# Kernel optimization log

Measured on AMD Instinct MI355X. Metric: run time of the kernel, lower is better.

The kernel has to match this reference:

```python
import jax, jax.numpy as jnp
import numpy as np
from jax.scipy.special import gammaln

REG = 0.1  # reg_param from __init__


def setup_inputs() -> dict:
    key = jax.random.key(0)
    k1, k2 = jax.random.split(key)
    D, C, S, Q = 512, 64, 16, 2048  # feature_dim, n_way, shots, n_query
    X_support = jax.random.normal(k1, (C * S, D), dtype=jnp.float32)
    # balanced class labels (equivalent to argmax of a one-hot y)
    labels = jnp.arange(C * S, dtype=jnp.int32) % C
    X_query = jax.random.normal(k2, (Q, D), dtype=jnp.float32)
    # learned parameters, initialized exactly as in the torch module
    m = jnp.zeros((1, D), dtype=jnp.float32)
    kappa = jnp.asarray(0.1, dtype=jnp.float32)
    nu = jnp.asarray(float(D), dtype=jnp.float32)
    triu_diag = jnp.ones((D,), dtype=jnp.float32)
    triu_lower = jnp.eye(D, dtype=jnp.float32)
    return {"X_support": X_support, "labels": labels, "X_query": X_query,
            "m": m, "kappa": kappa, "nu": nu,
            "triu_diag": triu_diag, "triu_lower": triu_lower, "n_classes": 64}


def _forward(X_support, X_query, m, kappa, nu, triu_diag, triu_lower, labels, n_classes):
    N, D = X_support.shape
    C = int(n_classes)
    S = N // C  # balanced episode: N_j == S for every class

    # lower_triu = diag(|triu_diag|) + triu_lower * strictly_lower_mask
    mask = jnp.tril(jnp.ones((D, D), dtype=X_support.dtype), -1)
    L = jnp.diag(jnp.abs(triu_diag)) + triu_lower * mask

    kap = jnp.abs(kappa) + 1e-6
    nu_ = jnp.clip(nu, D - 1 + 1e-6)

    # group support samples by class: [C, S, D] (stable sort keeps per-class order)
    order = jnp.argsort(labels)
    Xg = X_support[order].reshape(C, S, D)
    Xmean = Xg.mean(axis=1)  # [C, D]

    # posterior means mu_j = kappa/(kappa+N) m + N/(kappa+N) mean(X_j)
    mu = (kap / (kap + S)) * m + (S / (kap + S)) * Xmean  # [C, D]

    # sum_outer(X_j) as one batched GEMM instead of a per-row loop
    XtX = jnp.einsum('csd,cse->cde', Xg, Xg)  # [C, D, D]
    base = L @ L.T + kap * (m.T @ m)          # [D, D], shared across classes
    S_ns = base[None] + XtX - (kap + S) * jnp.einsum('cd,ce->cde', mu, mu)
    sigma = S_ns * ((kap + S + 1.0) / ((nu_ + S - D + 1.0) * (kap + S)))  # [C, D, D]

    eye = jnp.eye(D, dtype=sigma.dtype)
    sigma_inv = (1.0 - REG) * jnp.linalg.inv(sigma) + REG * eye  # regularize()

    common = nu_ + S + 1.0 - D  # scalar (equal shots per class)
    _, logdet = jnp.linalg.slogdet(sigma)  # [C]
    bias = (gammaln(0.5 * (common + D)) - gammaln(0.5 * common)
            - 0.5 * D * jnp.log(common) - 0.5 * logdet)  # [C]

    # batched Mahalanobis distances: replaces nested python loops in predict()
    diff = X_query[None, :, :] - mu[:, None, :]              # [C, Q, D]
    t = jnp.einsum('cqd,cde->cqe', diff, sigma_inv)          # [C, Q, D]
    dist = jnp.sum(t * diff, axis=-1)                        # [C, Q]

    logits = bias[:, None] - 0.5 * (common + D) * jnp.log1p(dist / common)
    return logits.T  # [Q, C]


def reference(X_support, labels, X_query, m, kappa, nu, triu_diag, triu_lower, n_classes):
    return _forward(X_support, X_query, m, kappa, nu, triu_diag, triu_lower,
                    labels, n_classes)
```

## Files before the change

kernel.cpp:

```cpp
#include <hip/hip_runtime.h>
#include <math.h>

#define DD    512
#define CNUM  64
#define SHOTS 16
#define NSUP  1024
#define QNQ   2048
#define REGP  0.1f
#define XKS   4

typedef __attribute__((ext_vector_type(8))) short short8;
typedef __attribute__((ext_vector_type(4))) float f32x4;

__device__ __forceinline__ unsigned short f2bf(float f) {
  unsigned int u = __float_as_uint(f);
  unsigned int r = (u + 0x7fffu + ((u >> 16) & 1u)) >> 16;
  return (unsigned short)r;
}
__device__ __forceinline__ float bf2f(unsigned short h) {
  return __uint_as_float((unsigned int)h << 16);
}

static constexpr size_t OFF_W     = 0;
static constexpr size_t OFF_MU    = OFF_W     + 512*512;
static constexpr size_t OFF_Y     = OFF_MU    + 64*512;
static constexpr size_t OFF_Z     = OFF_Y     + 3136*512;
static constexpr size_t OFF_WM    = OFF_Z     + 3136;
static constexpr size_t OFF_CONST = OFF_WM    + 512;
static constexpr size_t OFF_IDX   = OFF_CONST + 16;
static constexpr size_t OFF_RMAP  = OFF_IDX   + 1024;
static constexpr size_t OFF_ZG    = OFF_RMAP  + 1088;
static constexpr size_t OFF_VMU   = OFF_ZG    + 1088;
static constexpr size_t OFF_MUBMU = OFF_VMU   + 1088;
static constexpr size_t OFF_MUN   = OFF_MUBMU + 64;
static constexpr size_t OFF_MINV  = OFF_MUN   + 64;
static constexpr size_t OFF_BIAS  = OFF_MINV  + 64*289;
static constexpr size_t OFF_QNRM  = OFF_BIAS  + 64;
static constexpr size_t OFF_YN    = OFF_QNRM  + 2048;
static constexpr size_t OFF_XMU   = OFF_YN    + 2048;
static constexpr size_t OFF_RG    = OFF_XMU   + (size_t)XKS*2048*64;
static constexpr size_t OFF_P     = OFF_RG    + 1088*2048;
static constexpr size_t OFF_PX    = OFF_P     + 3136*512;
static constexpr size_t OFF_PW    = OFF_PX    + 3136*512;


__global__ __launch_bounds__(256) void f_init(const float* tdiag, const float* tlow,
    const float* kappa, const float* nu, const int* labels, const float* Xs,
    const float* Xq, const float* m, float* W, float* cst, int* idx,
    int* rowmap, float* mu, float* mun,
    unsigned short* PX, unsigned short* PW) {
  __shared__ float sh[2 * 64 * 68 + 32 * 33];
  __shared__ int sidx[SHOTS];
  int b = blockIdx.x, tid = threadIdx.x;
  if (b == 0) {
    if (tid == 0) {
      float kap = fabsf(kappa[0]) + 1e-6f;
      float nu_ = fmaxf(nu[0], (float)(DD - 1) + 1e-6f);
      float common = nu_ + (float)SHOTS + 1.0f - (float)DD;
      float scale = (kap + SHOTS + 1.0f) / ((nu_ + SHOTS - DD + 1.0f) * (kap + SHOTS));
      cst[0] = kap;
      cst[1] = scale;
      cst[2] = common;
      cst[3] = 0.5f * (common + DD);
      cst[4] = lgammaf(0.5f * (common + DD)) - lgammaf(0.5f * common)
               - 0.5f * (float)DD * logf(common);
      cst[5] = -(kap + SHOTS);
      cst[6] = kap / (kap + SHOTS);
      cst[7] = 1.0f / (kap + SHOTS);
      cst[8] = (float)DD * logf(scale);
      cst[9] = -1.0f / (kap + SHOTS);
    }
  } else if (b < 65) {
    int c = b - 1;
    if (tid < 64) {
      int lane = tid, cnt = 0;
      for (int i0 = 0; i0 < NSUP; i0 += 64) {
        int lab = labels[i0 + lane];
        unsigned long long mm = __ballot(lab == c);
        if (lab == c) {
          int pos = cnt + __popcll(mm & ((1ull << lane) - 1ull));
          if (pos < SHOTS) idx[c * SHOTS + pos] = i0 + lane;
        }
        cnt += __popcll(mm);
      }
    }
    __syncthreads();
    if (tid < 17)
      rowmap[c * 17 + tid] = (tid < SHOTS) ? (QNQ + idx[c * SHOTS + tid])
                                           : (QNQ + NSUP + c);
  } else if (b < 129) {
    int c = b - 65;
    if (tid < 64) {
      int lane = tid, cnt = 0;
      for (int i0 = 0; i0 < NSUP; i0 += 64) {
        int lab = labels[i0 + lane];
        unsigned long long mm = __ballot(lab == c);
        if (lab == c) {
          int pos = cnt + __popcll(mm & ((1ull << lane) - 1ull));
          if (pos < SHOTS) sidx[pos] = i0 + lane;
        }
        cnt += __popcll(mm);
      }
    }
    __syncthreads();
    float kap = fabsf(kappa[0]) + 1e-6f;
    float cm = kap / (kap + SHOTS), cx = 1.0f / (kap + SHOTS);
    float* red = sh;
    float acc = 0.0f;
    size_t prow = (size_t)(3072 + c) * 1024;
    for (int d = tid; d < DD; d += 256) {
      float s = 0.0f;
      for (int sh_ = 0; sh_ < SHOTS; sh_++)
        s += Xs[(size_t)sidx[sh_] * DD + d];
      float v = cm * m[d] + cx * s;
      mu[(size_t)c * DD + d] = v;
      unsigned short h = f2bf(v), l = f2bf(v - bf2f(h));
      PX[prow + d] = h;
      PX[prow + 512 + d] = l;
      acc += v * v;
    }
    red[tid] = acc;
    __syncthreads();
    for (int off = 128; off > 0; off >>= 1) {
      if (tid < off) red[tid] += red[tid + off];
      __syncthreads();
    }
    if (tid == 0) mun[c] = red[0];
  } else if (b < 137) {
    int jb = b - 129;
    float* Ld = sh;
    float* Wd = sh + 64 * 68;
    float* tsh = sh + 2 * 64 * 68;
    for (int t = tid; t < 4096; t += 256) {
      int r = t >> 6, c = t & 63;
      int gr = jb * 64 + r;
      float v = (r == c) ? fabsf(tdiag[gr])
              : (r > c ? tlow[(size_t)gr * DD + jb * 64 + c] : 0.0f);
      Ld[r * 68 + c] = v;
      Wd[r * 68 + c] = 0.0f;
    }
    __syncthreads();
    if (tid < 64) {
      int s = tid >> 4, t = tid & 15;
      int r0 = s * 16;
      #pragma unroll
      for (int i = 0; i < 16; i++) {
        float w = (i == t) ? 1.0f : 0.0f;
        #pragma unroll
        for (int k = 0; k < 16; k++)
          if (k < i) w -= Ld[(r0 + i) * 68 + r0 + k] * Wd[(r0 + k) * 68 + r0 + t];
        Wd[(r0 + i) * 68 + r0 + t] = w / Ld[(r0 + i) * 68 + r0 + i];
      }
    }
    __syncthreads();
    for (int g2 = 0; g2 < 2; g2++) {
      int r0 = g2 * 32 + 16, c0 = g2 * 32;
      int rr = tid >> 4, cc = tid & 15;
      float t_ = 0.0f;
      #pragma unroll
      for (int k = 0; k < 16; k++)
        t_ += Ld[(r0 + rr) * 68 + c0 + k] * Wd[(c0 + k) * 68 + c0 + cc];
      tsh[rr * 33 + cc] = t_;
      __syncthreads();
      float x = 0.0f;
      #pragma unroll
      for (int k = 0; k < 16; k++)
        x -= Wd[(r0 + rr) * 68 + r0 + k] * tsh[k * 33 + cc];
      Wd[(r0 + rr) * 68 + c0 + cc] = x;
      __syncthreads();
    }
    {
      int rr = tid >> 6, cc = tid & 63;
      #pragma unroll
      for (int p = 0; p < 4; p++) {
        int r = rr + p * 4, c = cc;
        if (c < 32) {
          float t_ = 0.0f;
          #pragma unroll
          for (int k = 0; k < 32; k++)
            t_ += Ld[(32 + r) * 68 + k] * Wd[k * 68 + c];
          tsh[r * 33 + c] = t_;
        } else {
          int c2 = c - 32;
          float t_ = 0.0f;
          #pragma unroll
          for (int k = 0; k < 32; k++)
            t_ += Ld[(32 + r + 16) * 68 + k] * Wd[k * 68 + c2];
          tsh[(r + 16) * 33 + c2] = t_;
        }
      }
      __syncthreads();
      #pragma unroll
      for (int p = 0; p < 4; p++) {
        int r = rr + p * 4, c = cc;
        int r2 = (c < 32) ? r : r + 16;
        int c2 = (c < 32) ? c : c - 32;
        float x = 0.0f;
        #pragma unroll
        for (int k = 0; k < 32; k++)
          x -= Wd[(32 + r2) * 68 + 32 + k] * tsh[k * 33 + c2];
        Wd[(32 + r2) * 68 + c2] = x;
      }
    }
    __syncthreads();
    float* Wblk = W + (size_t)(jb * 64) * DD + jb * 64;
    for (int t = tid; t < 4096; t += 256) {
      int r = t >> 6, c = t & 63;
      float v = Wd[r * 68 + c];
      Wblk[(size_t)r * DD + c] = v;
      unsigned short h = f2bf(v), l = f2bf(v - bf2f(h));
      size_t prow = (size_t)(jb * 64 + r) * 1024 + jb * 64 + c;
      PW[prow] = h;
      PW[prow + 512] = l;
    }
  } else {
    int r0 = (b - 137) * 4;
    int row = r0 + (tid >> 6), lane = tid & 63;
    const float* src = (row < QNQ) ? Xq + (size_t)row * DD
                                   : Xs + (size_t)(row - QNQ) * DD;
    size_t prow = (size_t)row * 1024;
    #pragma unroll
    for (int p = 0; p < 2; p++) {
      int col = lane * 8 + p * 4;
      float4 v = *(const float4*)(src + col);
      ushort4 hi, lo;
      hi.x = f2bf(v.x); lo.x = f2bf(v.x - bf2f(hi.x));
      hi.y = f2bf(v.y); lo.y = f2bf(v.y - bf2f(hi.y));
      hi.z = f2bf(v.z); lo.z = f2bf(v.z - bf2f(hi.z));
      hi.w = f2bf(v.w); lo.w = f2bf(v.w - bf2f(hi.w));
      *(ushort4*)(PX + prow + col) = hi;
      *(ushort4*)(PX + prow + 512 + col) = lo;
    }
  }
}

__device__ __forceinline__ void tile_stage(float* S, const float* __restrict__ G, int ldg) {
  int tid = threadIdx.x;
  #pragma unroll
  for (int p = 0; p < 4; p++) {
    int f4 = tid + 256 * p;
    int row = f4 >> 4, c4 = (f4 & 15) * 4;
    *(float4*)&S[row * 68 + c4] = *(const float4*)(G + (size_t)row * ldg + c4);
  }
}
__device__ __forceinline__ void tile_fma(float acc[4][4], const float* As, const float* Bs) {
  int tid = threadIdx.x, tr = tid >> 4, tc = tid & 15;
  #pragma unroll
  for (int kk = 0; kk < 64; kk++) {
    float a[4];
    #pragma unroll
    for (int x = 0; x < 4; x++) a[x] = As[(tr * 4 + x) * 68 + kk];
    float4 bv = *(const float4*)&Bs[kk * 68 + tc * 4];
    float bb[4] = {bv.x, bv.y, bv.z, bv.w};
    #pragma unroll
    for (int x = 0; x < 4; x++)
      #pragma unroll
      for (int y = 0; y < 4; y++) acc[x][y] += a[x] * bb[y];
  }
}
__device__ __forceinline__ void tile_out_neg(const float acc[4][4], float* W,
    unsigned short* PW, int gr0, int gc0) {
  int tid = threadIdx.x, tr = tid >> 4, tc = tid & 15;
  #pragma unroll
  for (int x = 0; x < 4; x++) {
    #pragma unroll
    for (int y = 0; y < 4; y++) {
      float v = -acc[x][y];
      W[(size_t)(gr0 + tr * 4 + x) * DD + gc0 + tc * 4 + y] = v;
      unsigned short h = f2bf(v), l = f2bf(v - bf2f(h));
      size_t prow = (size_t)(gr0 + tr * 4 + x) * 1024 + gc0 + tc * 4 + y;
      PW[prow] = h;
      PW[prow + 512] = l;
    }
  }
}

#define GBK 16
__global__ __launch_bounds__(256) void k_m128_xmu(const float* __restrict__ tlow,
    const float* __restrict__ W_, float* __restrict__ Wout,
    const float* __restrict__ Xq, const float* __restrict__ Mu,
    float* __restrict__ xmup, unsigned short* __restrict__ PW) {
  __shared__ float sh[3 * 64 * 68];
  int b = blockIdx.x, tid = threadIdx.x;
  if (b < 4) {
    float* As = sh;
    float* Bs = sh + 64 * 68;
    float* tsh = sh + 2 * 64 * 68;
    int base = b * 128;
    float tacc[4][4] = {};
    tile_stage(As, tlow + (size_t)(base + 64) * DD + base, DD);
    tile_stage(Bs, W_ + (size_t)base * DD + base, DD);
    __syncthreads();
    tile_fma(tacc, As, Bs);
    __syncthreads();
    {
      int tr = tid >> 4, tc = tid & 15;
      #pragma unroll
      for (int x = 0; x < 4; x++)
        #pragma unroll
        for (int y = 0; y < 4; y++) tsh[(tr * 4 + x) * 68 + tc * 4 + y] = tacc[x][y];
    }
    tile_stage(As, W_ + (size_t)(base + 64) * DD + base + 64, DD);
    __syncthreads();
    float xacc[4][4] = {};
    tile_fma(xacc, As, tsh);
    tile_out_neg(xacc, Wout, PW, base + 64, base);
  } else {
    float* Ms = sh;
    float* Qs = sh + 64 * 68;
    int xb = b - 4;
    int bm = (xb & 63) * 32, kq = xb >> 6;
    int tr = tid >> 4, tc = tid & 15;
    float acc[4][2] = {};
    int k0s = kq * (DD / XKS), k0e = k0s + DD / XKS;
    for (int k0 = k0s; k0 < k0e; k0 += GBK) {
      {
        int row = tid >> 2, k4 = tid & 3;
        float4 v = *(const float4*)(Mu + (size_t)row * DD + k0 + k4 * 4);
        Ms[(k4 * 4 + 0) * 68 + row] = v.x; Ms[(k4 * 4 + 1) * 68 + row] = v.y;
        Ms[(k4 * 4 + 2) * 68 + row] = v.z; Ms[(k4 * 4 + 3) * 68 + row] = v.w;
      }
      if (tid < 128) {
        int row = tid >> 2, k4 = tid & 3;
        float4 v = *(const float4*)(Xq + (size_t)(bm + row) * DD + k0 + k4 * 4);
        Qs[(k4 * 4 + 0) * 36 + row] = v.x; Qs[(k4 * 4 + 1) * 36 + row] = v.y;
        Qs[(k4 * 4 + 2) * 36 + row] = v.z; Qs[(k4 * 4 + 3) * 36 + row] = v.w;
      }
      __syncthreads();
      #pragma unroll
      for (int kk = 0; kk < GBK; kk++) {
        float4 m0 = *(const float4*)&Ms[kk * 68 + tr * 4];
        float a[4] = {m0.x, m0.y, m0.z, m0.w};
        float q0 = Qs[kk * 36 + tc * 2], q1 = Qs[kk * 36 + tc * 2 + 1];
        #pragma unroll
        for (int y = 0; y < 4; y++) {
          acc[y][0] += a[y] * q0;
          acc[y][1] += a[y] * q1;
        }
      }
      __syncthreads();
    }
    #pragma unroll
    for (int y = 0; y < 4; y++) {
      float2 v = make_float2(acc[y][0], acc[y][1]);
      *(float2*)(xmup + ((size_t)kq * CNUM + tr * 4 + y) * QNQ + bm + tc * 2) = v;
    }
  }
}

__global__ __launch_bounds__(256) void k_m256(const float* __restrict__ tlow,
    float* __restrict__ W, unsigned short* __restrict__ PW) {
  __shared__ float sh[3 * 64 * 68];
  float* As = sh;
  float* Bs = sh + 64 * 68;
  float* tsh = sh + 2 * 64 * 68;
  int b = blockIdx.x, tid = threadIdx.x;
  int g = b >> 2, rem = b & 3, i = rem >> 1, j = rem & 1;
  int base = g * 256;
  float xacc[4][4] = {};
  for (int k = 0; k <= i; k++) {
    float tacc[4][4] = {};
    for (int l = j; l < 2; l++) {
      __syncthreads();
      tile_stage(As, tlow + (size_t)(base + 128 + 64 * k) * DD + base + 64 * l, DD);
      tile_stage(Bs, W + (size_t)(base + 64 * l) * DD + base + 64 * j, DD);
      __syncthreads();
      tile_fma(tacc, As, Bs);
    }
    __syncthreads();
    {
      int tr = tid >> 4, tc = tid & 15;
      #pragma unroll
      for (int x = 0; x < 4; x++)
        #pragma unroll
        for (int y = 0; y < 4; y++) tsh[(tr * 4 + x) * 68 + tc * 4 + y] = tacc[x][y];
    }
    tile_stage(As, W + (size_t)(base + 128 + 64 * i) * DD + base + 128 + 64 * k, DD);
    __syncthreads();
    tile_fma(xacc, As, tsh);
  }
  tile_out_neg(xacc, W, PW, base + 128 + 64 * i, base + 64 * j);
}

__device__ __forceinline__ void nn64_sh(float* As, float* Bs,
    const float* __restrict__ A, int lda, const float* __restrict__ B, int ldb,
    float* __restrict__ Cd, int ldc, int k0, int k1, float sgn,
    unsigned short* __restrict__ Pw, int gr0, int gc0) {
  int tid = threadIdx.x, tr = tid >> 4, tc = tid & 15;
  float acc[4][4] = {};
  for (int kc = k0; kc < k1; kc += 64) {
    #pragma unroll
    for (int p = 0; p < 4; p++) {
      int f4 = tid + 256 * p;
      int row = f4 >> 4, c4 = f4 & 15;
      *(float4*)&As[row * 68 + c4 * 4] = *(const float4*)(A + (size_t)row * lda + kc + c4 * 4);
      *(float4*)&Bs[row * 68 + c4 * 4] = *(const float4*)(B + (size_t)(kc + row) * ldb + c4 * 4);
    }
    __syncthreads();
    #pragma unroll
    for (int kk = 0; kk < 64; kk++) {
      float a[4];
      #pragma unroll
      for (int x = 0; x < 4; x++) a[x] = As[(tr * 4 + x) * 68 + kk];
      float4 bv = *(const float4*)&Bs[kk * 68 + tc * 4];
      float bb[4] = {bv.x, bv.y, bv.z, bv.w};
      #pragma unroll
      for (int x = 0; x < 4; x++)
        #pragma unroll
        for (int y = 0; y < 4; y++) acc[x][y] += a[x] * bb[y];
    }
    __syncthreads();
  }
  #pragma unroll
  for (int x = 0; x < 4; x++) {
    float4 v = make_float4(sgn * acc[x][0], sgn * acc[x][1],
                           sgn * acc[x][2], sgn * acc[x][3]);
    *(float4*)(Cd + (size_t)(tr * 4 + x) * ldc + tc * 4) = v;
    if (Pw) {
      size_t prow = (size_t)(gr0 + tr * 4 + x) * 1024 + gc0 + tc * 4;
      float vv[4] = {v.x, v.y, v.z, v.w};
      #pragma unroll
      for (int y = 0; y < 4; y++) {
        unsigned short h = f2bf(vv[y]), l = f2bf(vv[y] - bf2f(h));
        Pw[prow + y] = h;
        Pw[prow + 512 + y] = l;
      }
    }
  }
}

__global__ __launch_bounds__(256) void k_triT(const float* __restrict__ tlow,
                                              const float* __restrict__ W,
                                              float* __restrict__ T, int s) {
  __shared__ float sh[2 * 64 * 68];
  int h = s >> 1, tiles = h >> 6, per = tiles * tiles;
  int g = blockIdx.x / per, rem = blockIdx.x % per;
  int ti = rem / tiles, tj = rem % tiles;
  int base = g * s;
  const float* A = tlow + (size_t)(base + h + ti * 64) * DD + base;
  const float* B = W + (size_t)base * DD + base + tj * 64;
  float* Cd = T + (size_t)g * h * h + (size_t)(ti * 64) * h + tj * 64;
  nn64_sh(sh, sh + 64 * 68, A, DD, B, DD, Cd, h, tj * 64, h, 1.0f, nullptr, 0, 0);
}

__global__ __launch_bounds__(256) void k_triX(float* __restrict__ W,
                                              const float* __restrict__ T, int s,
                                              unsigned short* __restrict__ PW) {
  __shared__ float sh[2 * 64 * 68];
  int h = s >> 1, tiles = h >> 6, per = tiles * tiles;
  int g = blockIdx.x / per, rem = blockIdx.x % per;
  int ti = rem / tiles, tj = rem % tiles;
  int base = g * s;
  const float* A = W + (size_t)(base + h + ti * 64) * DD + base + h;
  const float* B = T + (size_t)g * h * h + tj * 64;
  int gr0 = base + h + ti * 64, gc0 = base + tj * 64;
  float* Cd = W + (size_t)gr0 * DD + gc0;
  nn64_sh(sh, sh + 64 * 68, A, DD, B, h, Cd, DD, 0, (ti + 1) * 64, -1.0f, PW, gr0, gc0);
}

#define PSTR 80
__global__ __launch_bounds__(256) void f_y_wm(const unsigned short* __restrict__ PX,
    const unsigned short* __restrict__ PW, const float* __restrict__ W,
    const float* __restrict__ m, float* __restrict__ Y,
    unsigned short* __restrict__ Pm, float* __restrict__ wm) {
  __shared__ unsigned short AshH[64 * PSTR];
  __shared__ unsigned short AshL[64 * PSTR];
  __shared__ unsigned short BshH[64 * PSTR];
  __shared__ unsigned short BshL[64 * PSTR];
  int b = blockIdx.x, tid = threadIdx.x;
  if (b < 392) {
    int mt = b >> 3, nt = b & 7;
    int bm = mt * 64, bn = nt * 64;
    int lane = tid & 63, wave = tid >> 6;
    int wr = wave >> 1, wc = wave & 1;
    int mrow = lane & 15, q = lane >> 4;
    f32x4 acc00 = {}, acc01 = {}, acc10 = {}, acc11 = {};
    int kchunks = nt + 1;
    for (int it = 0; it < kchunks; it++) {
      int kc = it * 64;
      #pragma unroll
      for (int p = 0; p < 2; p++) {
        int idx = tid + 256 * p;
        int row = idx >> 3, c8 = (idx & 7) * 8;
        *(short8*)&AshH[row * PSTR + c8] =
            *(const short8*)(PX + (size_t)(bm + row) * 1024 + kc + c8);
        *(short8*)&AshL[row * PSTR + c8] =
            *(const short8*)(PX + (size_t)(bm + row) * 1024 + 512 + kc + c8);
        *(short8*)&BshH[row * PSTR + c8] =
            *(const short8*)(PW + (size_t)(bn + row) * 1024 + kc + c8);
        *(short8*)&BshL[row * PSTR + c8] =
            *(const short8*)(PW + (size_t)(bn + row) * 1024 + 512 + kc + c8);
      }
      __syncthreads();
      #pragma unroll
      for (int ks = 0; ks < 2; ks++) {
        int ko = ks * 32 + q * 8;
        short8 ah0 = *(const short8*)&AshH[(wr * 32 + mrow) * PSTR + ko];
        short8 ah1 = *(const short8*)&AshH[(wr * 32 + 16 + mrow) * PSTR + ko];
        short8 al0 = *(const short8*)&AshL[(wr * 32 + mrow) * PSTR + ko];
        short8 al1 = *(const short8*)&AshL[(wr * 32 + 16 + mrow) * PSTR + ko];
        short8 bh0 = *(const short8*)&BshH[(wc * 32 + mrow) * PSTR + ko];
        short8 bh1 = *(const short8*)&BshH[(wc * 32 + 16 + mrow) * PSTR + ko];
        short8 bl0 = *(const short8*)&BshL[(wc * 32 + mrow) * PSTR + ko];
        short8 bl1 = *(const short8*)&BshL[(wc * 32 + 16 + mrow) * PSTR + ko];
        acc00 = __builtin_amdgcn_mfma_f32_16x16x32_bf16(ah0, bh0, acc00, 0, 0, 0);
        acc00 = __builtin_amdgcn_mfma_f32_16x16x32_bf16(ah0, bl0, acc00, 0, 0, 0);
        acc00 = __builtin_amdgcn_mfma_f32_16x16x32_bf16(al0, bh0, acc00, 0, 0, 0);
        acc00 = __builtin_amdgcn_mfma_f32_16x16x32_bf16(al0, bl0, acc00, 0, 0, 0);
        acc01 = __builtin_amdgcn_mfma_f32_16x16x32_bf16(ah0, bh1, acc01, 0, 0, 0);
        acc01 = __builtin_amdgcn_mfma_f32_16x16x32_bf16(ah0, bl1, acc01, 0, 0, 0);
        acc01 = __builtin_amdgcn_mfma_f32_16x16x32_bf16(al0, bh1, acc01, 0, 0, 0);
        acc01 = __builtin_amdgcn_mfma_f32_16x16x32_bf16(al0, bl1, acc01, 0, 0, 0);
        acc10 = __builtin_amdgcn_mfma_f32_16x16x32_bf16(ah1, bh0, acc10, 0, 0, 0);
        acc10 = __builtin_amdgcn_mfma_f32_16x16x32_bf16(ah1, bl0, acc10, 0, 0, 0);
        acc10 = __builtin_amdgcn_mfma_f32_16x16x32_bf16(al1, bh0, acc10, 0, 0, 0);
        acc10 = __builtin_amdgcn_mfma_f32_16x16x32_bf16(al1, bl0, acc10, 0, 0, 0);
        acc11 = __builtin_amdgcn_mfma_f32_16x16x32_bf16(ah1, bh1, acc11, 0, 0, 0);
        acc11 = __builtin_amdgcn_mfma_f32_16x16x32_bf16(ah1, bl1, acc11, 0, 0, 0);
        acc11 = __builtin_amdgcn_mfma_f32_16x16x32_bf16(al1, bh1, acc11, 0, 0, 0);
        acc11 = __builtin_amdgcn_mfma_f32_16x16x32_bf16(al1, bl1, acc11, 0, 0, 0);
      }
      __syncthreads();
    }
    #pragma unroll
    for (int r = 0; r < 4; r++) {
      int row0 = bm + wr * 32 + q * 4 + r;
      int row1 = row0 + 16;
      int col0 = bn + wc * 32 + mrow;
      float vv[4] = {acc00[r], acc01[r], acc10[r], acc11[r]};
      int rows[4] = {row0, row0, row1, row1};
      int cols[4] = {col0, col0 + 16, col0, col0 + 16};
      #pragma unroll
      for (int e = 0; e < 4; e++) {
        Y[(size_t)rows[e] * DD + cols[e]] = vv[e];
        unsigned short h = f2bf(vv[e]), l = f2bf(vv[e] - bf2f(h));
        Pm[(size_t)rows[e] * 1024 + cols[e]] = h;
        Pm[(size_t)rows[e] * 1024 + 512 + cols[e]] = l;
      }
    }
  } else {
    int wave = tid >> 6, lane = tid & 63;
    int row = (b - 392) * 4 + wave;
    float s = 0.0f;
    for (int j = lane; j <= row; j += 64) s += W[(size_t)row * DD + j] * m[j];
    for (int off = 32; off > 0; off >>= 1) s += __shfl_down(s, off);
    if (lane == 0) wm[row] = s;
  }
}

__global__ __launch_bounds__(256) void f_z_rg_gram(const unsigned short* __restrict__ Pm,
    const float* __restrict__ Y, const float* __restrict__ tdiag,
    const int* __restrict__ rowmap, const float* __restrict__ Xq,
    const float* __restrict__ wm, float* __restrict__ cst,
    float* __restrict__ Rg,
    float* __restrict__ z, float* __restrict__ qn, float* __restrict__ yn,
    float* __restrict__ zg, float* __restrict__ Vmu, float* __restrict__ muBmu,
    float* __restrict__ Minv, float* __restrict__ bias) {
  __shared__ float sh[9920];
  __shared__ int pivrow;
  __shared__ float detacc, csmS, ldbS;
  int b = blockIdx.x, tid = threadIdx.x;
  if (b < 544) {
    unsigned short* ush = (unsigned short*)sh;
    unsigned short* Ash = ush;
    unsigned short* Bsh = ush + 64 * PSTR;
    unsigned short* Csh = ush + 2 * 64 * PSTR;
    int bm = (b >> 5) * 64, bn = (b & 31) * 64;
    int lane = tid & 63, wave = tid >> 6;
    int wr = wave >> 1, wc = wave & 1;
    int mrow = lane & 15, q = lane >> 4;
    int srowA[2];
    #pragma unroll
    for (int p = 0; p < 2; p++) srowA[p] = rowmap[bm + ((tid + 256 * p) >> 3)];
    f32x4 acc00 = {}, acc01 = {}, acc10 = {}, acc11 = {};
    for (int it = 0; it < 16; it++) {
      int kc = it * 64;
      int kcX = kc ^ 512;
      #pragma unroll
      for (int p = 0; p < 2; p++) {
        int idx = tid + 256 * p;
        int row = idx >> 3, c8 = (idx & 7) * 8;
        *(short8*)&Ash[row * PSTR + c8] =
            *(const short8*)(Pm + (size_t)srowA[p] * 1024 + kc + c8);
        *(short8*)&Bsh[row * PSTR + c8] =
            *(const short8*)(Pm + (size_t)(bn + row) * 1024 + kc + c8);
        *(short8*)&Csh[row * PSTR + c8] =
            *(const short8*)(Pm + (size_t)(bn + row) * 1024 + kcX + c8);
      }
      __syncthreads();
      #pragma unroll
      for (int ks = 0; ks < 2; ks++) {
        int ko = ks * 32 + q * 8;
        short8 a0 = *(const short8*)&Ash[(wr * 32 + mrow) * PSTR + ko];
        short8 a1 = *(const short8*)&Ash[(wr * 32 + 16 + mrow) * PSTR + ko];
        short8 b0 = *(const short8*)&Bsh[(wc * 32 + mrow) * PSTR + ko];
        short8 b1 = *(const short8*)&Bsh[(wc * 32 + 16 + mrow) * PSTR + ko];
        short8 c0 = *(const short8*)&Csh[(wc * 32 + mrow) * PSTR + ko];
        short8 c1 = *(const short8*)&Csh[(wc * 32 + 16 + mrow) * PSTR + ko];
        acc00 = __builtin_amdgcn_mfma_f32_16x16x32_bf16(a0, b0, acc00, 0, 0, 0);
        acc01 = __builtin_amdgcn_mfma_f32_16x16x32_bf16(a0, b1, acc01, 0, 0, 0);
        acc10 = __builtin_amdgcn_mfma_f32_16x16x32_bf16(a1, b0, acc10, 0, 0, 0);
        acc11 = __builtin_amdgcn_mfma_f32_16x16x32_bf16(a1, b1, acc11, 0, 0, 0);
        acc00 = __builtin_amdgcn_mfma_f32_16x16x32_bf16(a0, c0, acc00, 0, 0, 0);
        acc01 = __builtin_amdgcn_mfma_f32_16x16x32_bf16(a0, c1, acc01, 0, 0, 0);
        acc10 = __builtin_amdgcn_mfma_f32_16x16x32_bf16(a1, c0, acc10, 0, 0, 0);
        acc11 = __builtin_amdgcn_mfma_f32_16x16x32_bf16(a1, c1, acc11, 0, 0, 0);
      }
      __syncthreads();
    }
    #pragma unroll
    for (int r = 0; r < 4; r++) {
      int row0 = bm + wr * 32 + q * 4 + r;
      int row1 = row0 + 16;
      int col0 = bn + wc * 32 + mrow;
      Rg[(size_t)row0 * QNQ + col0]      = acc00[r];
      Rg[(size_t)row0 * QNQ + col0 + 16] = acc01[r];
      Rg[(size_t)row1 * QNQ + col0]      = acc10[r];
      Rg[(size_t)row1 * QNQ + col0 + 16] = acc11[r];
    }
  } else if (b < 1056) {
    int wave = tid >> 6, lane = tid & 63;
    int row = (b - 544) * 4 + wave;
    const float* xr = Xq + (size_t)row * DD;
    const float* yr = Y + (size_t)row * DD;
    float sz = 0.0f, s1 = 0.0f, s2 = 0.0f;
    for (int j4 = lane; j4 < 128; j4 += 64) {
      float4 xv = *(const float4*)(xr + j4 * 4);
      float4 yv = *(const float4*)(yr + j4 * 4);
      float4 wv = *(const float4*)(wm + j4 * 4);
      sz += yv.x * wv.x + yv.y * wv.y + yv.z * wv.z + yv.w * wv.w;
      s1 += xv.x * xv.x + xv.y * xv.y + xv.z * xv.z + xv.w * xv.w;
      s2 += yv.x * yv.x + yv.y * yv.y + yv.z * yv.z + yv.w * yv.w;
    }
    for (int off = 32; off > 0; off >>= 1) {
      sz += __shfl_down(sz, off);
      s1 += __shfl_down(s1, off);
      s2 += __shfl_down(s2, off);
    }
    if (lane == 0) {
      z[row] = sz;
      qn[row] = s1;
      yn[row] = s2;
    }
  } else if (b == 1056) {
    float* red = sh;
    float* red2 = sh + 256;
    float a = 0.0f, l = 0.0f;
    for (int t = tid; t < DD; t += 256) {
      float w = wm[t]; a += w * w;
      l += logf(fabsf(tdiag[t]));
    }
    red[tid] = a; red2[tid] = l;
    __syncthreads();
    for (int off = 128; off > 0; off >>= 1) {
      if (tid < off) { red[tid] += red[tid + off]; red2[tid] += red2[tid + off]; }
      __syncthreads();
    }
    if (tid == 0) {
      float kap = cst[0], ss = red[0];
      cst[10] = kap / (1.0f + kap * ss);
      cst[11] = 2.0f * red2[0] + logf(1.0f + kap * ss);
    }
  } else {
    int c = b - 1057;
    float* red = sh;
    float* red2 = sh + 256;
    {
      float a = 0.0f, l = 0.0f;
      for (int t = tid; t < DD; t += 256) {
        float w = wm[t]; a += w * w;
        l += logf(fabsf(tdiag[t]));
      }
      red[tid] = a; red2[tid] = l;
      __syncthreads();
      for (int off = 128; off > 0; off >>= 1) {
        if (tid < off) { red[tid] += red[tid + off]; red2[tid] += red2[tid + off]; }
        __syncthreads();
      }
      if (tid == 0) {
        float kap = cst[0], ss = red[0];
        csmS = kap / (1.0f + kap * ss);
        ldbS = 2.0f * red2[0] + logf(1.0f + kap * ss);
      }
      __syncthreads();
    }
    float* Ys  = sh;
    float* aug = sh + 8772;
    float* zs  = aug + 595;
    float* colk = zs + 17;
    for (int t = tid; t < 17 * 128; t += 256) {
      int r = t >> 7, col = t & 127;
      *(float4*)&Ys[r * 516 + col * 4] =
          *(const float4*)(Y + (size_t)rowmap[c * 17 + r] * DD + col * 4);
    }
    __syncthreads();
    {
      int wave = tid >> 6, lane = tid & 63;
      for (int a = wave; a < 17; a += 4) {
        float s = 0.0f;
        for (int j = lane; j < DD; j += 64) s += Ys[a * 516 + j] * wm[j];
        for (int off = 32; off > 0; off >>= 1) s += __shfl_down(s, off);
        if (lane == 0) zs[a] = s;
      }
    }
    __syncthreads();
    float csm = csmS;
    for (int e = tid; e < 289; e += 256) {
      int a = e / 17, bb = e % 17;
      const float* ra = &Ys[a * 516];
      const float* rb = &Ys[bb * 516];
      float s = 0.0f;
      for (int k = 0; k < 128; k++) {
        float4 va = *(const float4*)&ra[k * 4];
        float4 vb = *(const float4*)&rb[k * 4];
        s += va.x * vb.x + va.y * vb.y + va.z * vb.z + va.w * vb.w;
      }
      float g = s - csm * zs[a] * zs[bb];
      if (a == bb) g += (a < 16) ? 1.0f : cst[9];
      aug[a * 35 + bb] = g;
      aug[a * 35 + 17 + bb] = (a == bb) ? 1.0f : 0.0f;
    }
    __syncthreads();
    if (tid < 17) {
      float gv = aug[tid * 35 + 16];
      if (tid == 16) gv -= cst[9];
      Vmu[c * 17 + tid] = gv;
      if (tid == 16) muBmu[c] = gv;
      zg[c * 17 + tid] = zs[tid];
    }
    if (tid == 0) detacc = 0.0f;
    __syncthreads();
    for (int k = 0; k < 17; k++) {
      if (tid == 0) {
        int p = k; float best = fabsf(aug[k * 35 + k]);
        for (int r = k + 1; r < 17; r++) {
          float v = fabsf(aug[r * 35 + k]);
          if (v > best) { best = v; p = r; }
        }
        pivrow = p;
      }
      __syncthreads();
      int p = pivrow;
      if (p != k) {
        for (int cc = tid; cc < 34; cc += 256) {
          float tmp = aug[k * 35 + cc]; aug[k * 35 + cc] = aug[p * 35 + cc]; aug[p * 35 + cc] = tmp;
        }
      }
      __syncthreads();
      if (tid == 0) detacc += logf(fabsf(aug[k * 35 + k]));
      if (tid < 17) colk[tid] = aug[tid * 35 + k];
      __syncthreads();
      float invp = 1.0f / aug[k * 35 + k];
      for (int cc = tid; cc < 34; cc += 256) aug[k * 35 + cc] *= invp;
      __syncthreads();
      for (int t = tid; t < 17 * 34; t += 256) {
        int r = t / 34, cc = t % 34;
        if (r != k) aug[r * 35 + cc] -= colk[r] * aug[k * 35 + cc];
      }
      __syncthreads();
    }
    for (int t = tid; t < 289; t += 256)
      Minv[(size_t)c * 289 + t] = aug[(t / 17) * 35 + 17 + t % 17];
    if (tid == 0) {
      float slog = logf(fabsf(cst[5])) + detacc;
      float logdetSigma = cst[8] + ldbS + slog;
      bias[c] = cst[4] - 0.5f * logdetSigma;
    }
  }
}

__global__ __launch_bounds__(256) void k_logits(const float* __restrict__ Rg,
    const float* z, const float* zg,
    const float* Vmu, const float* muBmu, const float* mun, const float* yn,
    const float* qn, const float* xmup, const float* Minv, const float* bias,
    const float* cst, float* out) {
  __shared__ float Ms[289], Vs[17], Zs[17];
  int c = blockIdx.y;
  int q = blockIdx.x * 256 + threadIdx.x;
  for (int t = threadIdx.x; t < 289; t += 256) Ms[t] = Minv[(size_t)c * 289 + t];
  if (threadIdx.x < 17) {
    Vs[threadIdx.x] = Vmu[c * 17 + threadIdx.x];
    Zs[threadIdx.x] = zg[c * 17 + threadIdx.x];
  }
  __syncthreads();
  float csm = cst[10], scale = cst[1], common = cst[2], coef = cst[3];
  float zq = z[q];
  float r[17];
  float xBmu = 0.0f;
  for (int a = 0; a < 17; a++) {
    float raw = Rg[(size_t)(c * 17 + a) * QNQ + q] - csm * Zs[a] * zq;
    if (a == 16) xBmu = raw;
    r[a] = raw - Vs[a];
  }
  float qB = yn[q] - csm * zq * zq;
  float quadB = qB - 2.0f * xBmu + muBmu[c];
  float corr = 0.0f;
  for (int a = 0; a < 17; a++) {
    float e = 0.0f;
    for (int bb = 0; bb < 17; bb++) e += Ms[a * 17 + bb] * r[bb];
    corr += r[a] * e;
  }
  float distB = (quadB - corr) / scale;
  float xm = 0.0f;
  #pragma unroll
  for (int p = 0; p < XKS; p++)
    xm += xmup[((size_t)(p * CNUM + c)) * QNQ + q];
  float dn = qn[q] - 2.0f * xm + mun[c];
  float dist = (1.0f - REGP) * distB + REGP * dn;
  out[(size_t)q * CNUM + c] = bias[c] - coef * log1pf(dist / common);
}

extern "C" void kernel_launch(void* const* d_in, const int* in_sizes, int n_in,
                              void* d_out, int out_size, void* d_ws, size_t ws_size,
                              hipStream_t stream) {
  const float* Xs    = (const float*)d_in[0];
  const int*   labels= (const int*)d_in[1];
  const float* Xq    = (const float*)d_in[2];
  const float* m     = (const float*)d_in[3];
  const float* kappa = (const float*)d_in[4];
  const float* nu    = (const float*)d_in[5];
  const float* tdiag = (const float*)d_in[6];
  const float* tlow  = (const float*)d_in[7];
  float* ws = (float*)d_ws;
  float* W    = ws + OFF_W;
  float* mu   = ws + OFF_MU;
  float* Y    = ws + OFF_Y;
  float* z    = ws + OFF_Z;
  float* wm   = ws + OFF_WM;
  float* cst  = ws + OFF_CONST;
  int*   idx  = (int*)(ws + OFF_IDX);
  int*   rmap = (int*)(ws + OFF_RMAP);
  float* zg   = ws + OFF_ZG;
  float* Vmu  = ws + OFF_VMU;
  float* muBmu= ws + OFF_MUBMU;
  float* mun  = ws + OFF_MUN;
  float* Minv = ws + OFF_MINV;
  float* bias = ws + OFF_BIAS;
  float* qn   = ws + OFF_QNRM;
  float* yn   = ws + OFF_YN;
  float* xmup = ws + OFF_XMU;
  float* Rg   = ws + OFF_RG;
  unsigned short* P  = (unsigned short*)(ws + OFF_P);
  unsigned short* PX = (unsigned short*)(ws + OFF_PX);
  unsigned short* PW = (unsigned short*)(ws + OFF_PW);
  float* Ttmp = ws + OFF_RG;
  float* out  = (float*)d_out;

  f_init<<<905, 256, 0, stream>>>(tdiag, tlow, kappa, nu, labels, Xs, Xq, m,
                                  W, cst, idx, rmap, mu, mun, PX, PW);
  k_m128_xmu<<<260, 256, 0, stream>>>(tlow, W, W, Xq, mu, xmup, PW);
  k_m256<<<8, 256, 0, stream>>>(tlow, W, PW);
  k_triT<<<16, 256, 0, stream>>>(tlow, W, Ttmp, 512);
  k_triX<<<16, 256, 0, stream>>>(W, Ttmp, 512, PW);
  f_y_wm<<<520, 256, 0, stream>>>(PX, PW, W, m, Y, P, wm);
  f_z_rg_gram<<<544 + 512 + 1 + 64, 256, 0, stream>>>(P, Y, tdiag, rmap, Xq, wm,
                                                      cst, Rg, z, qn, yn,
                                                      zg, Vmu, muBmu, Minv, bias);
  k_logits<<<dim3(QNQ / 256, CNUM), 256, 0, stream>>>(Rg, z, zg, Vmu, muBmu,
                                                      mun, yn, qn, xmup, Minv, bias,
                                                      cst, out);
  (void)in_sizes; (void)n_in; (void)out_size; (void)ws_size;
}
```

Before: 203.6 us.

## Move per-class 17x17 Gauss-Jordan into one wave and schedule those blocks first

The 64 per-class blocks, which build a small Gram matrix and invert it with pivoted Gauss-Jordan, now run first in the fused grid instead of last, so the long serial tail can overlap with the GEMM and row-norm blocks. The inversion is redone inside a single wavefront, with each lane holding one column in registers and using shuffles, which removes the many __syncthreads barriers per pivot step. The Gram matrix is computed only over its symmetric lower triangle and mirrored, and block-wide reductions are replaced with wave shuffle reductions. The costs are a larger register footprint (17 floats per lane for the column) and three idle waves during the inversion.

```diff
diff --git a/kernel.cpp b/kernel.cpp
--- a/kernel.cpp
+++ b/kernel.cpp
@@ -557,15 +557,153 @@
     float* __restrict__ zg, float* __restrict__ Vmu, float* __restrict__ muBmu,
     float* __restrict__ Minv, float* __restrict__ bias) {
   __shared__ float sh[9920];
-  __shared__ int pivrow;
-  __shared__ float detacc, csmS, ldbS;
+  __shared__ float csmS;
   int b = blockIdx.x, tid = threadIdx.x;
-  if (b < 544) {
+  if (b < 64) {
+    int c = b;
+    int lane = tid & 63, wave = tid >> 6;
+    float* Ys  = sh;
+    float* aug = sh + 8772;
+    float* zsv = aug + 306;
+    float kap = cst[0], cst9 = cst[9];
+    for (int t = tid; t < 17 * 128; t += 256) {
+      int r = t >> 7, col = t & 127;
+      *(float4*)&Ys[r * 516 + col * 4] =
+          *(const float4*)(Y + (size_t)rowmap[c * 17 + r] * DD + col * 4);
+    }
+    float ldb_r = 0.0f;
+    if (wave == 0) {
+      float aa = 0.0f, ll = 0.0f;
+      for (int t = lane; t < DD; t += 64) {
+        float w = wm[t]; aa += w * w;
+        ll += logf(fabsf(tdiag[t]));
+      }
+      #pragma unroll
+      for (int off = 32; off > 0; off >>= 1) {
+        aa += __shfl_xor(aa, off);
+        ll += __shfl_xor(ll, off);
+      }
+      ldb_r = 2.0f * ll + logf(1.0f + kap * aa);
+      if (lane == 0) csmS = kap / (1.0f + kap * aa);
+    }
+    __syncthreads();
+    if (wave > 0) {
+      for (int a = wave - 1; a < 17; a += 3) {
+        float s = 0.0f;
+        for (int j = lane; j < 128; j += 64) {
+          float4 yv = *(const float4*)&Ys[a * 516 + j * 4];
+          float4 wv = *(const float4*)(wm + j * 4);
+          s += yv.x * wv.x + yv.y * wv.y + yv.z * wv.z + yv.w * wv.w;
+        }
+        #pragma unroll
+        for (int off = 32; off > 0; off >>= 1) s += __shfl_xor(s, off);
+        if (lane == 0) zsv[a] = s;
+      }
+    }
+    __syncthreads();
+    float csm = csmS;
+    for (int e = tid; e < 153; e += 256) {
+      int a = (int)((sqrtf(8.0f * (float)e + 1.0f) - 1.0f) * 0.5f);
+      while (((a + 1) * (a + 2)) / 2 <= e) a++;
+      while ((a * (a + 1)) / 2 > e) a--;
+      int bb = e - (a * (a + 1)) / 2;
+      const float* ra = &Ys[a * 516];
+      const float* rb = &Ys[bb * 516];
+      float s = 0.0f;
+      for (int k = 0; k < 128; k++) {
+        float4 va = *(const float4*)&ra[k * 4];
+        float4 vb = *(const float4*)&rb[k * 4];
+        s += va.x * vb.x + va.y * vb.y + va.z * vb.z + va.w * vb.w;
+      }
+      float g = s - csm * zsv[a] * zsv[bb];
+      if (a == bb) g += (a < 16) ? 1.0f : cst9;
+      aug[a * 18 + bb] = g;
+      if (a != bb) aug[bb * 18 + a] = g;
+    }
+    __syncthreads();
+    if (wave == 0) {
+      float colv[17];
+      bool left = lane < 17;
+      bool right = (lane >= 17 && lane < 34);
+      #pragma unroll
+      for (int r = 0; r < 17; r++) {
+        float lv = aug[r * 18 + (lane & 31)];
+        colv[r] = left ? lv : ((right && (lane - 17) == r) ? 1.0f : 0.0f);
+      }
+      float det = 0.0f;
+      #pragma unroll
+      for (int k = 0; k < 17; k++) {
+        float best = fabsf(colv[k]); int bp = k;
+        #pragma unroll
+        for (int r = k + 1; r < 17; r++) {
+          float v = fabsf(colv[r]);
+          if (v > best) { best = v; bp = r; }
+        }
+        int p = __shfl(bp, k);
+        float pv = colv[k];
+        #pragma unroll
+        for (int r = k + 1; r < 17; r++) pv = (p == r) ? colv[r] : pv;
+        float oldk = colv[k];
+        #pragma unroll
+        for (int r = k + 1; r < 17; r++) colv[r] = (p == r) ? oldk : colv[r];
+        colv[k] = pv;
+        float piv = __shfl(pv, k);
+        if (lane == 0) det += logf(fabsf(piv));
+        float invp = 1.0f / piv;
+        float rk = pv * invp;
+        colv[k] = rk;
+        #pragma unroll
+        for (int r = 0; r < 17; r++) {
+          if (r == k) continue;
+          float ck = __shfl(colv[r], k);
+          colv[r] = fmaf(-ck, rk, colv[r]);
+        }
+      }
+      if (right) {
+        int bb = lane - 17;
+        #pragma unroll
+        for (int r = 0; r < 17; r++)
+          Minv[(size_t)c * 289 + r * 17 + bb] = colv[r];
+      }
+      if (lane == 0) {
+        float slog = logf(fabsf(cst[5])) + det;
+        float logdetSigma = cst[8] + ldb_r + slog;
+        bias[c] = cst[4] - 0.5f * logdetSigma;
+      }
+    } else if (wave == 1) {
+      if (lane < 17) {
+        float gv = aug[lane * 18 + 16];
+        if (lane == 16) gv -= cst9;
+        Vmu[c * 17 + lane] = gv;
+        if (lane == 16) muBmu[c] = gv;
+        zg[c * 17 + lane] = zsv[lane];
+      }
+    }
+  } else if (b == 64) {
+    if (tid < 64) {
+      float aa = 0.0f, ll = 0.0f;
+      for (int t = tid; t < DD; t += 64) {
+        float w = wm[t]; aa += w * w;
+        ll += logf(fabsf(tdiag[t]));
+      }
+      #pragma unroll
+      for (int off = 32; off > 0; off >>= 1) {
+        aa += __shfl_xor(aa, off);
+        ll += __shfl_xor(ll, off);
+      }
+      if (tid == 0) {
+        float kap = cst[0];
+        cst[10] = kap / (1.0f + kap * aa);
+        cst[11] = 2.0f * ll + logf(1.0f + kap * aa);
+      }
+    }
+  } else if (b < 609) {
     unsigned short* ush = (unsigned short*)sh;
     unsigned short* Ash = ush;
     unsigned short* Bsh = ush + 64 * PSTR;
     unsigned short* Csh = ush + 2 * 64 * PSTR;
-    int bm = (b >> 5) * 64, bn = (b & 31) * 64;
+    int rb = b - 65;
+    int bm = (rb >> 5) * 64, bn = (rb & 31) * 64;
     int lane = tid & 63, wave = tid >> 6;
     int wr = wave >> 1, wc = wave & 1;
     int mrow = lane & 15, q = lane >> 4;
@@ -618,9 +756,9 @@
       Rg[(size_t)row1 * QNQ + col0]      = acc10[r];
       Rg[(size_t)row1 * QNQ + col0 + 16] = acc11[r];
     }
-  } else if (b < 1056) {
+  } else {
     int wave = tid >> 6, lane = tid & 63;
-    int row = (b - 544) * 4 + wave;
+    int row = (b - 609) * 4 + wave;
     const float* xr = Xq + (size_t)row * DD;
     const float* yr = Y + (size_t)row * DD;
     float sz = 0.0f, s1 = 0.0f, s2 = 0.0f;
@@ -641,130 +779,6 @@
       z[row] = sz;
       qn[row] = s1;
       yn[row] = s2;
-    }
-  } else if (b == 1056) {
-    float* red = sh;
-    float* red2 = sh + 256;
-    float a = 0.0f, l = 0.0f;
-    for (int t = tid; t < DD; t += 256) {
-      float w = wm[t]; a += w * w;
-      l += logf(fabsf(tdiag[t]));
-    }
-    red[tid] = a; red2[tid] = l;
-    __syncthreads();
-    for (int off = 128; off > 0; off >>= 1) {
-      if (tid < off) { red[tid] += red[tid + off]; red2[tid] += red2[tid + off]; }
-      __syncthreads();
-    }
-    if (tid == 0) {
-      float kap = cst[0], ss = red[0];
-      cst[10] = kap / (1.0f + kap * ss);
-      cst[11] = 2.0f * red2[0] + logf(1.0f + kap * ss);
-    }
-  } else {
-    int c = b - 1057;
-    float* red = sh;
-    float* red2 = sh + 256;
-    {
-      float a = 0.0f, l = 0.0f;
-      for (int t = tid; t < DD; t += 256) {
-        float w = wm[t]; a += w * w;
-        l += logf(fabsf(tdiag[t]));
-      }
-      red[tid] = a; red2[tid] = l;
-      __syncthreads();
-      for (int off = 128; off > 0; off >>= 1) {
-        if (tid < off) { red[tid] += red[tid + off]; red2[tid] += red2[tid + off]; }
-        __syncthreads();
-      }
-      if (tid == 0) {
-        float kap = cst[0], ss = red[0];
-        csmS = kap / (1.0f + kap * ss);
-        ldbS = 2.0f * red2[0] + logf(1.0f + kap * ss);
-      }
-      __syncthreads();
-    }
-    float* Ys  = sh;
-    float* aug = sh + 8772;
-    float* zs  = aug + 595;
-    float* colk = zs + 17;
-    for (int t = tid; t < 17 * 128; t += 256) {
-      int r = t >> 7, col = t & 127;
-      *(float4*)&Ys[r * 516 + col * 4] =
-          *(const float4*)(Y + (size_t)rowmap[c * 17 + r] * DD + col * 4);
-    }
-    __syncthreads();
-    {
-      int wave = tid >> 6, lane = tid & 63;
-      for (int a = wave; a < 17; a += 4) {
-        float s = 0.0f;
-        for (int j = lane; j < DD; j += 64) s += Ys[a * 516 + j] * wm[j];
-        for (int off = 32; off > 0; off >>= 1) s += __shfl_down(s, off);
-        if (lane == 0) zs[a] = s;
-      }
-    }
-    __syncthreads();
-    float csm = csmS;
-    for (int e = tid; e < 289; e += 256) {
-      int a = e / 17, bb = e % 17;
-      const float* ra = &Ys[a * 516];
-      const float* rb = &Ys[bb * 516];
-      float s = 0.0f;
-      for (int k = 0; k < 128; k++) {
-        float4 va = *(const float4*)&ra[k * 4];
-        float4 vb = *(const float4*)&rb[k * 4];
-        s += va.x * vb.x + va.y * vb.y + va.z * vb.z + va.w * vb.w;
-      }
-      float g = s - csm * zs[a] * zs[bb];
-      if (a == bb) g += (a < 16) ? 1.0f : cst[9];
-      aug[a * 35 + bb] = g;
-      aug[a * 35 + 17 + bb] = (a == bb) ? 1.0f : 0.0f;
-    }
-    __syncthreads();
-    if (tid < 17) {
-      float gv = aug[tid * 35 + 16];
-      if (tid == 16) gv -= cst[9];
-      Vmu[c * 17 + tid] = gv;
-      if (tid == 16) muBmu[c] = gv;
-      zg[c * 17 + tid] = zs[tid];
-    }
-    if (tid == 0) detacc = 0.0f;
-    __syncthreads();
-    for (int k = 0; k < 17; k++) {
-      if (tid == 0) {
-        int p = k; float best = fabsf(aug[k * 35 + k]);
-        for (int r = k + 1; r < 17; r++) {
-          float v = fabsf(aug[r * 35 + k]);
-          if (v > best) { best = v; p = r; }
-        }
-        pivrow = p;
-      }
-      __syncthreads();
-      int p = pivrow;
-      if (p != k) {
-        for (int cc = tid; cc < 34; cc += 256) {
-          float tmp = aug[k * 35 + cc]; aug[k * 35 + cc] = aug[p * 35 + cc]; aug[p * 35 + cc] = tmp;
-        }
-      }
-      __syncthreads();
-      if (tid == 0) detacc += logf(fabsf(aug[k * 35 + k]));
-      if (tid < 17) colk[tid] = aug[tid * 35 + k];
-      __syncthreads();
-      float invp = 1.0f / aug[k * 35 + k];
-      for (int cc = tid; cc < 34; cc += 256) aug[k * 35 + cc] *= invp;
-      __syncthreads();
-      for (int t = tid; t < 17 * 34; t += 256) {
-        int r = t / 34, cc = t % 34;
-        if (r != k) aug[r * 35 + cc] -= colk[r] * aug[k * 35 + cc];
-      }
-      __syncthreads();
-    }
-    for (int t = tid; t < 289; t += 256)
-      Minv[(size_t)c * 289 + t] = aug[(t / 17) * 35 + 17 + t % 17];
-    if (tid == 0) {
-      float slog = logf(fabsf(cst[5])) + detacc;
-      float logdetSigma = cst[8] + ldbS + slog;
-      bias[c] = cst[4] - 0.5f * logdetSigma;
     }
   }
 }
@@ -853,7 +867,7 @@
   k_triT<<<16, 256, 0, stream>>>(tlow, W, Ttmp, 512);
   k_triX<<<16, 256, 0, stream>>>(W, Ttmp, 512, PW);
   f_y_wm<<<520, 256, 0, stream>>>(PX, PW, W, m, Y, P, wm);
-  f_z_rg_gram<<<544 + 512 + 1 + 64, 256, 0, stream>>>(P, Y, tdiag, rmap, Xq, wm,
+  f_z_rg_gram<<<64 + 1 + 544 + 512, 256, 0, stream>>>(P, Y, tdiag, rmap, Xq, wm,
                                                       cst, Rg, z, qn, yn,
                                                       zg, Vmu, muBmu, Minv, bias);
   k_logits<<<dim3(QNQ / 256, CNUM), 256, 0, stream>>>(Rg, z, zg, Vmu, muBmu,
```

Result: faster. 189.1 us (-7.1%).
